# Optimization experiments

Hardware: AMD Instinct MI355X
Metric: run time of the kernel (lower is better)

The kernel has to match this reference:

```python
import jax, jax.numpy as jnp
import numpy as np

H = 8          # num_heads
L = 256        # lifting_dim
DH = L // H    # head dim


def setup_inputs() -> dict:
    key = jax.random.key(0)
    ks = jax.random.split(key, 32)
    B, N, E = 4, 16384, 65536
    Dn, De, Dg = 128, 64, 32

    def lin_w(k, din, dout):
        return jax.random.normal(k, (din, dout), jnp.float32) * (din ** -0.5)

    inp = {
        "node_features": jax.random.normal(ks[0], (B, N, Dn), jnp.float32),
        "edge_features": jax.random.normal(ks[1], (B, E, De), jnp.float32),
        "energy": jax.random.normal(ks[2], (Dg,), jnp.float32),
        "W_node": lin_w(ks[3], Dn, L), "b_node": jnp.zeros((L,), jnp.float32),
        "W_edge": lin_w(ks[4], De, L), "b_edge": jnp.zeros((L,), jnp.float32),
        "W_graph": lin_w(ks[5], Dg, L), "b_graph": jnp.zeros((L,), jnp.float32),
        "Wq": lin_w(ks[6], L, L), "bq": jnp.zeros((L,), jnp.float32),
        # stacked per-hetero-type key/value projections: [3, L, L]
        "Wk": jnp.stack([lin_w(ks[7 + i], L, L) for i in range(3)]),
        "bk": jnp.zeros((3, L), jnp.float32),
        "Wv": jnp.stack([lin_w(ks[10 + i], L, L) for i in range(3)]),
        "bv": jnp.zeros((3, L), jnp.float32),
        "W_out": lin_w(ks[13], L, L), "b_out": jnp.zeros((L,), jnp.float32),
    }
    return inp


def _heads(x, B, T):
    # [B,T,L] -> [B,H,T,DH]
    return x.reshape(B, T, H, DH).transpose(0, 2, 1, 3)


def reference(node_features, edge_features, energy,
              W_node, b_node, W_edge, b_edge, W_graph, b_graph,
              Wq, bq, Wk, bk, Wv, bv, W_out, b_out):
    B, N, _ = node_features.shape
    lifted_nodes = node_features @ W_node + b_node            # [B,N,L]
    lifted_edges = edge_features @ W_edge + b_edge            # [B,E,L]
    lifted_graph = jnp.broadcast_to(energy, (B, 1, energy.shape[0])) @ W_graph + b_graph  # [B,1,L]

    hetero = [lifted_nodes, lifted_edges, lifted_graph]

    q = _heads(lifted_nodes @ Wq + bq, B, N)                  # [B,H,N,DH]
    q = jax.nn.softmax(q, axis=-1)

    out = None
    # NOTE: faithful to the original, `out` is overwritten each iteration,
    # so only the last hetero feature (graph) determines the output.
    for i in range(3):
        h = hetero[i]
        T = h.shape[1]
        k = jax.nn.softmax(_heads(h @ Wk[i] + bk[i], B, T), axis=-1)  # [B,H,T,DH]
        v = _heads(h @ Wv[i] + bv[i], B, T)                           # [B,H,T,DH]
        k_sum = k.sum(axis=-2, keepdims=True)                          # [B,H,1,DH]
        d_inv = 1.0 / jnp.clip((q * k_sum).sum(axis=-1, keepdims=True), 1e-8)  # [B,H,N,1]
        kv = jnp.einsum("bhtd,bhte->bhde", k, v)                       # [B,H,DH,DH]
        out = q + jnp.einsum("bhnd,bhde->bhne", q, kv) * d_inv         # [B,H,N,DH]

    out = out.transpose(0, 2, 1, 3).reshape(B, N, L)
    return out @ W_out + b_out
```

## Files before the change

kernel.cpp:

```cpp
#include <hip/hip_runtime.h>
#include <hip/hip_bf16.h>
#include <cstdint>
#include <cstddef>


typedef __attribute__((ext_vector_type(8))) short short8;
typedef __attribute__((ext_vector_type(4))) short short4v;
typedef __attribute__((ext_vector_type(4))) float floatx4;

using bf16 = __hip_bfloat16;

static constexpr int Mrows = 65536;
static constexpr int Lcols = 256;

static __device__ __forceinline__ short f2bs(float x) {
  bf16 h = __float2bfloat16(x);
  return *reinterpret_cast<short*>(&h);
}

__global__ void k_setup(const float* __restrict__ W_node,
                        const float* __restrict__ Wq,
                        const float* __restrict__ W_out,
                        const float* __restrict__ energy,
                        const float* __restrict__ W_graph,
                        const float* __restrict__ b_graph,
                        const float* __restrict__ Wk,
                        const float* __restrict__ bk,
                        const float* __restrict__ Wv,
                        const float* __restrict__ bv,
                        const float* __restrict__ b_node,
                        const float* __restrict__ bq,
                        short* __restrict__ wnq_t,
                        short* __restrict__ wto_t,
                        float* __restrict__ vvec,
                        float* __restrict__ bnq) {
  const int b = blockIdx.x;
  const int t = threadIdx.x;

  if (b < 256) {
    __shared__ float wqc[256];
    const int j = b;
    wqc[t] = Wq[t * 256 + j];
    __syncthreads();
    if (t < 128) {
      const float* wr = W_node + t * 256;
      float acc = 0.f;
#pragma unroll 8
      for (int l = 0; l < 256; ++l) acc += wr[l] * wqc[l];
      wnq_t[j * 128 + t] = f2bs(acc);
    }
  } else if (b < 512) {
    const int r = b - 256;
    wto_t[t * 256 + r] = f2bs(W_out[r * 256 + t]);
  } else {
    __shared__ float ev[32];
    __shared__ float lg[256];
    __shared__ float r1[256], r2[256];
    const int h = b - 512;
    if (t < 32) ev[t] = energy[t];
    __syncthreads();

    {
      float lgd = b_graph[t];
#pragma unroll
      for (int e = 0; e < 32; ++e) lgd += ev[e] * W_graph[e * 256 + t];
      lg[t] = lgd;
    }
    __syncthreads();

    const int g = t >> 5;
    const int c = t & 31;
    const int j = h * 32 + c;
    float p1 = 0.f, p2 = 0.f;
#pragma unroll
    for (int i = 0; i < 32; ++i) {
      const int d = g * 32 + i;
      p1 += lg[d] * Wv[2 * 65536 + d * 256 + j];
      p2 += b_node[d] * Wq[d * 256 + j];
    }
    r1[t] = p1; r2[t] = p2;
    __syncthreads();
    if (t < 32) {
      float s1 = 0.f, s2 = 0.f;
#pragma unroll
      for (int gg = 0; gg < 8; ++gg) {
        s1 += r1[gg * 32 + c]; s2 += r2[gg * 32 + c];
      }
      vvec[j] = s1 + bv[512 + j];
      bnq[j]  = s2 + bq[j];
    }
  }
}

__global__ __launch_bounds__(256, 4)
void k_fused(const float* __restrict__ nf,
             const short* __restrict__ wnq,
             const short* __restrict__ wto,
             const float* __restrict__ bnq,
             const float* __restrict__ vvec,
             const float* __restrict__ b_out,
             float* __restrict__ out) {
  constexpr int AS_STR = 136;
  constexpr int PS_STR = 264;
  __shared__ short smem[64 * PS_STR];

  const int t = threadIdx.x;
  const int lane = t & 63;
  const int l15 = lane & 15;
  const int lhi = lane >> 4;
  const int cw = (t >> 6) * 64;
  const int rowBase = blockIdx.x * 64;
  const int colq = cw + lhi * 4;

  {
    const int row = t >> 2;
    const int c0 = (t & 3) << 5;
    const float* src = nf + (size_t)(rowBase + row) * 128 + c0;
    short tmp[32];
#pragma unroll
    for (int i = 0; i < 8; ++i) {
      float4 f = *(const float4*)(src + i * 4);
      tmp[i * 4 + 0] = f2bs(f.x); tmp[i * 4 + 1] = f2bs(f.y);
      tmp[i * 4 + 2] = f2bs(f.z); tmp[i * 4 + 3] = f2bs(f.w);
    }
#pragma unroll
    for (int i = 0; i < 4; ++i)
      *(short8*)(&smem[row * AS_STR + c0 + i * 8]) = *(short8*)(&tmp[i * 8]);
  }

  const short* wb1 = wnq + (cw + l15) * 128 + lhi * 8;
  short8 pbf1[4];
#pragma unroll
  for (int n = 0; n < 4; ++n) pbf1[n] = *(const short8*)(wb1 + n * 16 * 128);
  floatx4 bnq4[4], vv4[4];
#pragma unroll
  for (int n = 0; n < 4; ++n) {
    bnq4[n] = *(const floatx4*)(&bnq[colq + n * 16]);
    vv4[n]  = *(const floatx4*)(&vvec[colq + n * 16]);
  }

  __syncthreads();

  floatx4 acc[4][4];
#pragma unroll
  for (int m = 0; m < 4; ++m)
#pragma unroll
    for (int n = 0; n < 4; ++n) acc[m][n] = (floatx4){0.f, 0.f, 0.f, 0.f};

  {
#pragma unroll
    for (int kc = 0; kc < 4; ++kc) {
      short8 af[4], bfv[4];
#pragma unroll
      for (int n = 0; n < 4; ++n)
        bfv[n] = (kc == 0) ? pbf1[n]
                           : *(const short8*)(wb1 + n * 16 * 128 + kc * 32);
#pragma unroll
      for (int m = 0; m < 4; ++m)
        af[m] = *(const short8*)(&smem[(m * 16 + l15) * AS_STR + kc * 32 + lhi * 8]);
#pragma unroll
      for (int m = 0; m < 4; ++m)
#pragma unroll
        for (int n = 0; n < 4; ++n)
          acc[m][n] = __builtin_amdgcn_mfma_f32_16x16x32_bf16(bfv[n], af[m],
                                                              acc[m][n], 0, 0, 0);
    }
  }

  const short* wb2 = wto + (cw + l15) * 256 + lhi * 8;
  short8 pbf2[4];
#pragma unroll
  for (int n = 0; n < 4; ++n) pbf2[n] = *(const short8*)(wb2 + n * 16 * 256);

  __syncthreads();

#pragma unroll
  for (int m = 0; m < 4; ++m) {
#pragma unroll
    for (int tt = 0; tt < 2; ++tt) {
      const int n0 = 2 * tt, n1 = n0 + 1;
      float e0[4], e1[4];
#pragma unroll
      for (int r = 0; r < 4; ++r) {
        e0[r] = __expf(acc[m][n0][r] + bnq4[n0][r]);
        e1[r] = __expf(acc[m][n1][r] + bnq4[n1][r]);
      }
      float s = ((e0[0] + e0[1]) + (e0[2] + e0[3]))
              + ((e1[0] + e1[1]) + (e1[2] + e1[3]));
      s += __shfl_xor(s, 16);
      s += __shfl_xor(s, 32);
      const float inv = 1.0f / s;
      short4v p0, p1;
#pragma unroll
      for (int r = 0; r < 4; ++r) {
        p0[r] = f2bs(e0[r] * inv + vv4[n0][r]);
        p1[r] = f2bs(e1[r] * inv + vv4[n1][r]);
      }
      const int prow = (m * 16 + l15) * PS_STR;
      *(short4v*)(&smem[prow + colq + n0 * 16]) = p0;
      *(short4v*)(&smem[prow + colq + n1 * 16]) = p1;
    }
  }
#pragma unroll
  for (int m = 0; m < 4; ++m)
#pragma unroll
    for (int n = 0; n < 4; ++n) acc[m][n] = (floatx4){0.f, 0.f, 0.f, 0.f};
  __syncthreads();

  {
#pragma unroll
    for (int kc = 0; kc < 8; ++kc) {
      short8 af[4], bfv[4];
#pragma unroll
      for (int n = 0; n < 4; ++n)
        bfv[n] = (kc == 0) ? pbf2[n]
                           : *(const short8*)(wb2 + n * 16 * 256 + kc * 32);
#pragma unroll
      for (int m = 0; m < 4; ++m)
        af[m] = *(const short8*)(&smem[(m * 16 + l15) * PS_STR + kc * 32 + lhi * 8]);
#pragma unroll
      for (int m = 0; m < 4; ++m)
#pragma unroll
        for (int n = 0; n < 4; ++n)
          acc[m][n] = __builtin_amdgcn_mfma_f32_16x16x32_bf16(bfv[n], af[m],
                                                              acc[m][n], 0, 0, 0);
    }
  }

  floatx4 bo4[4];
#pragma unroll
  for (int n = 0; n < 4; ++n) bo4[n] = *(const floatx4*)(&b_out[colq + n * 16]);

#pragma unroll
  for (int m = 0; m < 4; ++m) {
    const size_t rbase = (size_t)(rowBase + m * 16 + l15) * Lcols;
#pragma unroll
    for (int n = 0; n < 4; ++n) {
      floatx4 v = acc[m][n] + bo4[n];
      *(floatx4*)(&out[rbase + colq + n * 16]) = v;
    }
  }
}

extern "C" void kernel_launch(void* const* d_in, const int* in_sizes, int n_in,
                              void* d_out, int out_size, void* d_ws, size_t ws_size,
                              hipStream_t stream) {
  const float* node_features = (const float*)d_in[0];
  const float* energy  = (const float*)d_in[2];
  const float* W_node  = (const float*)d_in[3];
  const float* b_node  = (const float*)d_in[4];
  const float* W_graph = (const float*)d_in[7];
  const float* b_graph = (const float*)d_in[8];
  const float* Wq      = (const float*)d_in[9];
  const float* bq      = (const float*)d_in[10];
  const float* Wk      = (const float*)d_in[11];
  const float* bk      = (const float*)d_in[12];
  const float* Wv      = (const float*)d_in[13];
  const float* bv      = (const float*)d_in[14];
  const float* W_out   = (const float*)d_in[15];
  const float* b_out   = (const float*)d_in[16];

  char* ws = (char*)d_ws;
  short* wnq_t = (short*)(ws);
  short* wto_t = (short*)(ws + 65536);
  float* vvec  = (float*)(ws + 196608);
  float* bnq   = (float*)(ws + 197632);

  k_setup<<<dim3(520), dim3(256), 0, stream>>>(
      W_node, Wq, W_out, energy, W_graph, b_graph, Wk, bk, Wv, bv,
      b_node, bq, wnq_t, wto_t, vvec, bnq);

  k_fused<<<dim3(Mrows / 64), dim3(256), 0, stream>>>(
      node_features, wnq_t, wto_t, bnq, vvec, b_out, (float*)d_out);
}
```

Baseline: 193.2 us.

## Load node features straight into MFMA fragments and stage output stores through LDS

After: 202.4 us. 4.7% more time.

```diff
diff --git a/kernel.cpp b/kernel.cpp
--- a/kernel.cpp
+++ b/kernel.cpp
@@ -100,9 +100,10 @@
              const float* __restrict__ vvec,
              const float* __restrict__ b_out,
              float* __restrict__ out) {
-  constexpr int AS_STR = 136;
   constexpr int PS_STR = 264;
+  constexpr int FO_STR = 260;
   __shared__ short smem[64 * PS_STR];
+  float* fsm = (float*)smem;
 
   const int t = threadIdx.x;
   const int lane = t & 63;
@@ -112,34 +113,17 @@
   const int rowBase = blockIdx.x * 64;
   const int colq = cw + lhi * 4;
 
-  {
-    const int row = t >> 2;
-    const int c0 = (t & 3) << 5;
-    const float* src = nf + (size_t)(rowBase + row) * 128 + c0;
-    short tmp[32];
-#pragma unroll
-    for (int i = 0; i < 8; ++i) {
-      float4 f = *(const float4*)(src + i * 4);
-      tmp[i * 4 + 0] = f2bs(f.x); tmp[i * 4 + 1] = f2bs(f.y);
-      tmp[i * 4 + 2] = f2bs(f.z); tmp[i * 4 + 3] = f2bs(f.w);
-    }
-#pragma unroll
-    for (int i = 0; i < 4; ++i)
-      *(short8*)(&smem[row * AS_STR + c0 + i * 8]) = *(short8*)(&tmp[i * 8]);
-  }
+  const float* abase = nf + (size_t)(rowBase + l15) * 128 + lhi * 8;
 
   const short* wb1 = wnq + (cw + l15) * 128 + lhi * 8;
-  short8 pbf1[4];
-#pragma unroll
-  for (int n = 0; n < 4; ++n) pbf1[n] = *(const short8*)(wb1 + n * 16 * 128);
-  floatx4 bnq4[4], vv4[4];
+  const short* wb2 = wto + (cw + l15) * 256 + lhi * 8;
+  floatx4 bnq4[4], vv4[4], bo4[4];
 #pragma unroll
   for (int n = 0; n < 4; ++n) {
     bnq4[n] = *(const floatx4*)(&bnq[colq + n * 16]);
     vv4[n]  = *(const floatx4*)(&vvec[colq + n * 16]);
-  }
-
-  __syncthreads();
+    bo4[n]  = *(const floatx4*)(&b_out[colq + n * 16]);
+  }
 
   floatx4 acc[4][4];
 #pragma unroll
@@ -153,11 +137,17 @@
       short8 af[4], bfv[4];
 #pragma unroll
       for (int n = 0; n < 4; ++n)
-        bfv[n] = (kc == 0) ? pbf1[n]
-                           : *(const short8*)(wb1 + n * 16 * 128 + kc * 32);
-#pragma unroll
-      for (int m = 0; m < 4; ++m)
-        af[m] = *(const short8*)(&smem[(m * 16 + l15) * AS_STR + kc * 32 + lhi * 8]);
+        bfv[n] = *(const short8*)(wb1 + n * 16 * 128 + kc * 32);
+#pragma unroll
+      for (int m = 0; m < 4; ++m) {
+        const float* ap = abase + m * 16 * 128 + kc * 32;
+        float4 f0 = *(const float4*)(ap);
+        float4 f1 = *(const float4*)(ap + 4);
+        af[m][0] = f2bs(f0.x); af[m][1] = f2bs(f0.y);
+        af[m][2] = f2bs(f0.z); af[m][3] = f2bs(f0.w);
+        af[m][4] = f2bs(f1.x); af[m][5] = f2bs(f1.y);
+        af[m][6] = f2bs(f1.z); af[m][7] = f2bs(f1.w);
+      }
 #pragma unroll
       for (int m = 0; m < 4; ++m)
 #pragma unroll
@@ -167,12 +157,9 @@
     }
   }
 
-  const short* wb2 = wto + (cw + l15) * 256 + lhi * 8;
   short8 pbf2[4];
 #pragma unroll
   for (int n = 0; n < 4; ++n) pbf2[n] = *(const short8*)(wb2 + n * 16 * 256);
-
-  __syncthreads();
 
 #pragma unroll
   for (int m = 0; m < 4; ++m) {
@@ -204,7 +191,7 @@
 #pragma unroll
   for (int m = 0; m < 4; ++m)
 #pragma unroll
-    for (int n = 0; n < 4; ++n) acc[m][n] = (floatx4){0.f, 0.f, 0.f, 0.f};
+    for (int n = 0; n < 4; ++n) acc[m][n] = bo4[n];
   __syncthreads();
 
   {
@@ -227,17 +214,25 @@
     }
   }
 
-  floatx4 bo4[4];
-#pragma unroll
-  for (int n = 0; n < 4; ++n) bo4[n] = *(const floatx4*)(&b_out[colq + n * 16]);
-
-#pragma unroll
-  for (int m = 0; m < 4; ++m) {
-    const size_t rbase = (size_t)(rowBase + m * 16 + l15) * Lcols;
-#pragma unroll
-    for (int n = 0; n < 4; ++n) {
-      floatx4 v = acc[m][n] + bo4[n];
-      *(floatx4*)(&out[rbase + colq + n * 16]) = v;
+#pragma unroll
+  for (int c = 0; c < 2; ++c) {
+    __syncthreads();
+#pragma unroll
+    for (int mm = 0; mm < 2; ++mm) {
+      const int m = c * 2 + mm;
+      const int frow = (mm * 16 + l15) * FO_STR;
+#pragma unroll
+      for (int n = 0; n < 4; ++n)
+        *(floatx4*)(&fsm[frow + colq + n * 16]) = acc[m][n];
+    }
+    __syncthreads();
+#pragma unroll
+    for (int i = 0; i < 8; ++i) {
+      const int f = i * 256 + t;
+      const int row = f >> 6;
+      const int c4 = (f & 63) << 2;
+      float4 vv = *(const float4*)(&fsm[row * FO_STR + c4]);
+      *(float4*)(&out[(size_t)(rowBase + c * 32 + row) * Lcols + c4]) = vv;
     }
   }
 }
```

## Stage output through LDS for coalesced stores and prefetch more weight fragments

Applied to the files above, without the earlier changes.

Measured after the change: 185.8 us. -3.8%, faster.

```diff
diff --git a/kernel.cpp b/kernel.cpp
--- a/kernel.cpp
+++ b/kernel.cpp
@@ -92,7 +92,7 @@
   }
 }
 
-__global__ __launch_bounds__(256, 4)
+__global__ __launch_bounds__(256, 2)
 void k_fused(const float* __restrict__ nf,
              const short* __restrict__ wnq,
              const short* __restrict__ wto,
@@ -102,7 +102,9 @@
              float* __restrict__ out) {
   constexpr int AS_STR = 136;
   constexpr int PS_STR = 264;
+  constexpr int FO_STR = 260;
   __shared__ short smem[64 * PS_STR];
+  float* fsm = (float*)smem;
 
   const int t = threadIdx.x;
   const int lane = t & 63;
@@ -112,6 +114,9 @@
   const int rowBase = blockIdx.x * 64;
   const int colq = cw + lhi * 4;
 
+  const short* wb1 = wnq + (cw + l15) * 128 + lhi * 8;
+  const short* wb2 = wto + (cw + l15) * 256 + lhi * 8;
+
   {
     const int row = t >> 2;
     const int c0 = (t & 3) << 5;
@@ -128,49 +133,49 @@
       *(short8*)(&smem[row * AS_STR + c0 + i * 8]) = *(short8*)(&tmp[i * 8]);
   }
 
-  const short* wb1 = wnq + (cw + l15) * 128 + lhi * 8;
-  short8 pbf1[4];
-#pragma unroll
-  for (int n = 0; n < 4; ++n) pbf1[n] = *(const short8*)(wb1 + n * 16 * 128);
+  short8 pbf1[4][4];
+#pragma unroll
+  for (int kc = 0; kc < 4; ++kc)
+#pragma unroll
+    for (int n = 0; n < 4; ++n)
+      pbf1[kc][n] = *(const short8*)(wb1 + n * 16 * 128 + kc * 32);
+
+  __syncthreads();
+
+  floatx4 acc[4][4];
+#pragma unroll
+  for (int m = 0; m < 4; ++m)
+#pragma unroll
+    for (int n = 0; n < 4; ++n) acc[m][n] = (floatx4){0.f, 0.f, 0.f, 0.f};
+
+  {
+#pragma unroll
+    for (int kc = 0; kc < 4; ++kc) {
+      short8 af[4];
+#pragma unroll
+      for (int m = 0; m < 4; ++m)
+        af[m] = *(const short8*)(&smem[(m * 16 + l15) * AS_STR + kc * 32 + lhi * 8]);
+#pragma unroll
+      for (int m = 0; m < 4; ++m)
+#pragma unroll
+        for (int n = 0; n < 4; ++n)
+          acc[m][n] = __builtin_amdgcn_mfma_f32_16x16x32_bf16(pbf1[kc][n], af[m],
+                                                              acc[m][n], 0, 0, 0);
+    }
+  }
+
+  short8 pbf2[2][4];
+#pragma unroll
+  for (int kc = 0; kc < 2; ++kc)
+#pragma unroll
+    for (int n = 0; n < 4; ++n)
+      pbf2[kc][n] = *(const short8*)(wb2 + n * 16 * 256 + kc * 32);
   floatx4 bnq4[4], vv4[4];
 #pragma unroll
   for (int n = 0; n < 4; ++n) {
     bnq4[n] = *(const floatx4*)(&bnq[colq + n * 16]);
     vv4[n]  = *(const floatx4*)(&vvec[colq + n * 16]);
   }
-
-  __syncthreads();
-
-  floatx4 acc[4][4];
-#pragma unroll
-  for (int m = 0; m < 4; ++m)
-#pragma unroll
-    for (int n = 0; n < 4; ++n) acc[m][n] = (floatx4){0.f, 0.f, 0.f, 0.f};
-
-  {
-#pragma unroll
-    for (int kc = 0; kc < 4; ++kc) {
-      short8 af[4], bfv[4];
-#pragma unroll
-      for (int n = 0; n < 4; ++n)
-        bfv[n] = (kc == 0) ? pbf1[n]
-                           : *(const short8*)(wb1 + n * 16 * 128 + kc * 32);
-#pragma unroll
-      for (int m = 0; m < 4; ++m)
-        af[m] = *(const short8*)(&smem[(m * 16 + l15) * AS_STR + kc * 32 + lhi * 8]);
-#pragma unroll
-      for (int m = 0; m < 4; ++m)
-#pragma unroll
-        for (int n = 0; n < 4; ++n)
-          acc[m][n] = __builtin_amdgcn_mfma_f32_16x16x32_bf16(bfv[n], af[m],
-                                                              acc[m][n], 0, 0, 0);
-    }
-  }
-
-  const short* wb2 = wto + (cw + l15) * 256 + lhi * 8;
-  short8 pbf2[4];
-#pragma unroll
-  for (int n = 0; n < 4; ++n) pbf2[n] = *(const short8*)(wb2 + n * 16 * 256);
 
   __syncthreads();
 
@@ -201,10 +206,13 @@
       *(short4v*)(&smem[prow + colq + n1 * 16]) = p1;
     }
   }
+  floatx4 bo4[4];
+#pragma unroll
+  for (int n = 0; n < 4; ++n) bo4[n] = *(const floatx4*)(&b_out[colq + n * 16]);
 #pragma unroll
   for (int m = 0; m < 4; ++m)
 #pragma unroll
-    for (int n = 0; n < 4; ++n) acc[m][n] = (floatx4){0.f, 0.f, 0.f, 0.f};
+    for (int n = 0; n < 4; ++n) acc[m][n] = bo4[n];
   __syncthreads();
 
   {
@@ -213,8 +221,8 @@
       short8 af[4], bfv[4];
 #pragma unroll
       for (int n = 0; n < 4; ++n)
-        bfv[n] = (kc == 0) ? pbf2[n]
-                           : *(const short8*)(wb2 + n * 16 * 256 + kc * 32);
+        bfv[n] = (kc < 2) ? pbf2[kc][n]
+                          : *(const short8*)(wb2 + n * 16 * 256 + kc * 32);
 #pragma unroll
       for (int m = 0; m < 4; ++m)
         af[m] = *(const short8*)(&smem[(m * 16 + l15) * PS_STR + kc * 32 + lhi * 8]);
@@ -227,17 +235,25 @@
     }
   }
 
-  floatx4 bo4[4];
-#pragma unroll
-  for (int n = 0; n < 4; ++n) bo4[n] = *(const floatx4*)(&b_out[colq + n * 16]);
-
-#pragma unroll
-  for (int m = 0; m < 4; ++m) {
-    const size_t rbase = (size_t)(rowBase + m * 16 + l15) * Lcols;
-#pragma unroll
-    for (int n = 0; n < 4; ++n) {
-      floatx4 v = acc[m][n] + bo4[n];
-      *(floatx4*)(&out[rbase + colq + n * 16]) = v;
+#pragma unroll
+  for (int c = 0; c < 2; ++c) {
+    __syncthreads();
+#pragma unroll
+    for (int mm = 0; mm < 2; ++mm) {
+      const int m = c * 2 + mm;
+      const int frow = (mm * 16 + l15) * FO_STR;
+#pragma unroll
+      for (int n = 0; n < 4; ++n)
+        *(floatx4*)(&fsm[frow + colq + n * 16]) = acc[m][n];
+    }
+    __syncthreads();
+#pragma unroll
+    for (int i = 0; i < 8; ++i) {
+      const int f = i * 256 + t;
+      const int row = f >> 6;
+      const int c4 = (f & 63) << 2;
+      float4 vv = *(const float4*)(&fsm[row * FO_STR + c4]);
+      *(float4*)(&out[(size_t)(rowBase + c * 32 + row) * Lcols + c4]) = vv;
     }
   }
 }
```
